# Performance work log

Hardware: AMD Instinct MI355X
Metric: run time of the kernel (lower is better)

The kernel has to match this reference:

```python
import jax, jax.numpy as jnp
import numpy as np

B, C, H, W = 4, 128, 96, 96
INTER = C // 2


def setup_inputs() -> dict:
    key = jax.random.key(0)
    ks = jax.random.split(key, 6)
    scale = 1.0 / np.sqrt(C)
    return {
        "x1": jax.random.normal(ks[0], (B, C, H, W), dtype=jnp.float32),
        "x2": jax.random.normal(ks[1], (B, C, H, W), dtype=jnp.float32),
        "w_theta": jax.random.normal(ks[2], (INTER, C), dtype=jnp.float32) * scale,
        "w_phi": jax.random.normal(ks[3], (INTER, C), dtype=jnp.float32) * scale,
        "w_g": jax.random.normal(ks[4], (INTER, C), dtype=jnp.float32) * scale,
        "w_mask": jax.random.normal(ks[5], (C, INTER), dtype=jnp.float32) * (1.0 / np.sqrt(INTER)),
    }


def reference(x1, x2, w_theta, w_phi, w_g, w_mask):
    b, c, h1, w1 = x1.shape  # c == full channel
    inter = c // 2
    # 1x1 convs (no bias) == channel GEMMs
    theta = jnp.einsum('ic,bchw->bihw', w_theta, x1)   # [b, inter, h1, w1]
    phi   = jnp.einsum('ic,bchw->bihw', w_phi,   x2)   # [b, inter, h2, w2]
    g     = jnp.einsum('ic,bchw->bihw', w_g,     x2)   # [b, inter, h2, w2]
    # Faithful to original: .view(b, c, -1) with c = FULL channel count,
    # so the flattened length is H*W/2 and the contraction dim is c (row-major reshape).
    theta = theta.reshape(b, c, -1).transpose(0, 2, 1)  # [b, N1, c], N1 = h1*w1//2
    phi = phi.reshape(b, c, -1)                         # [b, c, N2]
    g = g.reshape(b, c, -1).transpose(0, 2, 1)          # [b, N2, c]
    scores = jnp.einsum('bnc,bcm->bnm', theta, phi)     # [b, N1, N2]
    attn = jax.nn.softmax(scores, axis=1)               # softmax over dim=1 (query axis!)
    y = jnp.einsum('bnm,bmc->bnc', attn, g)             # [b, N1, c]
    y = y.transpose(0, 2, 1).reshape(b, inter, h1, w1)  # [b, inter, h1, w1]
    mask = jnp.einsum('ci,bihw->bchw', w_mask, y)       # [b, c, h1, w1]
    return mask + x1
```

## Files before the change

### kernel.cpp

```cpp
#include <hip/hip_runtime.h>

typedef __attribute__((ext_vector_type(8))) short short8;
typedef __attribute__((ext_vector_type(4))) float f32x4;
typedef __attribute__((ext_vector_type(16))) float f32x16;
typedef unsigned short u16;
typedef unsigned int u32;

#define NB 4
#define CH 128
#define INTER2 64
#define HW2 9216
#define NN 4608
#define NSLICE 8
#define SLW 576
#define SK 8
#define PCH 136

__device__ __forceinline__ u16 f2bf(float f) {
  u32 u = __float_as_uint(f);
  u += 0x7fffu + ((u >> 16) & 1u);
  return (u16)(u >> 16);
}
__device__ __forceinline__ float bf2f(u16 h) { return __uint_as_float(((u32)h) << 16); }
__device__ __forceinline__ u32 cvtpk(float lo, float hi) {
  u32 r;
  asm("v_cvt_pk_bf16_f32 %0, %1, %2" : "=v"(r) : "v"(lo), "v"(hi));
  return r;
}
__device__ __forceinline__ void gl_lds16(const u16* g, u16* l) {
  __builtin_amdgcn_global_load_lds(
      (const __attribute__((address_space(1))) unsigned int*)g,
      (__attribute__((address_space(3))) unsigned int*)l, 16, 0, 0);
}

__global__ void k_wcvt(const float* __restrict__ wt, const float* __restrict__ wp,
                       const float* __restrict__ wg, const float* __restrict__ wm,
                       u16* __restrict__ wtb, u16* __restrict__ wpb,
                       u16* __restrict__ wgb, u16* __restrict__ wmb) {
  int i = blockIdx.x * 256 + threadIdx.x;
  if (i < CH * INTER2) {
    wtb[i] = f2bf(wt[i]);
    wpb[i] = f2bf(wp[i]);
    wgb[i] = f2bf(wg[i]);
    wmb[i] = f2bf(wm[i]);
  }
}

__global__ __launch_bounds__(256) void k_conv(const float* __restrict__ x1,
                                              const float* __restrict__ x2,
                                              const u16* __restrict__ wtb,
                                              const u16* __restrict__ wpb,
                                              const u16* __restrict__ wgb,
                                              u16* __restrict__ Tt,
                                              u16* __restrict__ Pt,
                                              u16* __restrict__ Gn) {
  __shared__ u16 xT[64 * PCH];
  __shared__ u16 ot[64 * 72];
  const int tid = threadIdx.x;
  const int w = tid >> 6, l = tid & 63, lr = l & 15, lg = l >> 4;
  const int pt = blockIdx.x, b = blockIdx.y, z = blockIdx.z;
  const int p0 = pt * 64;
  const int h = (p0 >= NN) ? 1 : 0;
  const int n0 = p0 - h * NN;
  const float* X = (z ? x2 : x1) + (size_t)b * CH * HW2;

  {
    const int pq = (l & 15) * 4;
    const int cs = w + 4 * (l >> 4);
#pragma unroll
    for (int it = 0; it < 8; it++) {
      const int c = it * 16 + cs;
      float4 v = *(const float4*)(X + (size_t)c * HW2 + p0 + pq);
      xT[(pq + 0) * PCH + c] = f2bf(v.x);
      xT[(pq + 1) * PCH + c] = f2bf(v.y);
      xT[(pq + 2) * PCH + c] = f2bf(v.z);
      xT[(pq + 3) * PCH + c] = f2bf(v.w);
    }
  }
  short8 wsP[4], wsG[4];
  {
    const u16* W1 = z ? wpb : wtb;
#pragma unroll
    for (int ks = 0; ks < 4; ks++)
      wsP[ks] = *(const short8*)(W1 + (w * 16 + lr) * CH + ks * 32 + lg * 8);
    if (z) {
#pragma unroll
      for (int ks = 0; ks < 4; ks++)
        wsG[ks] = *(const short8*)(wgb + (w * 16 + lr) * CH + ks * 32 + lg * 8);
    }
  }
  __syncthreads();
  short8 xf[4][4];
#pragma unroll
  for (int tp = 0; tp < 4; tp++)
#pragma unroll
    for (int ks = 0; ks < 4; ks++)
      xf[tp][ks] = *(const short8*)(&xT[(tp * 16 + lr) * PCH + ks * 32 + lg * 8]);

  f32x4 accP[4];
#pragma unroll
  for (int tp = 0; tp < 4; tp++) {
#pragma unroll
    for (int j = 0; j < 4; j++) accP[tp][j] = 0.f;
#pragma unroll
    for (int ks = 0; ks < 4; ks++)
      accP[tp] = __builtin_amdgcn_mfma_f32_16x16x32_bf16(xf[tp][ks], wsP[ks], accP[tp], 0, 0, 0);
  }
#pragma unroll
  for (int tp = 0; tp < 4; tp++) {
#pragma unroll
    for (int j = 0; j < 4; j++)
      ot[(tp * 16 + lg * 4 + j) * 72 + w * 16 + lr] = f2bf(accP[tp][j]);
  }
  if (z) {
    f32x4 accG[4];
#pragma unroll
    for (int tp = 0; tp < 4; tp++) {
#pragma unroll
      for (int j = 0; j < 4; j++) accG[tp][j] = 0.f;
#pragma unroll
      for (int ks = 0; ks < 4; ks++)
        accG[tp] = __builtin_amdgcn_mfma_f32_16x16x32_bf16(wsG[ks], xf[tp][ks], accG[tp], 0, 0, 0);
    }
    u16* Gb = Gn + (size_t)b * CH * NN;
#pragma unroll
    for (int tp = 0; tp < 4; tp++) {
#pragma unroll
      for (int j = 0; j < 4; j++) {
        const int ig = w * 16 + lg * 4 + j;
        Gb[(size_t)((h << 6) + ig) * NN + n0 + tp * 16 + lr] = f2bf(accG[tp][j]);
      }
    }
  }
  __syncthreads();
  {
    u16* dst = (z ? Pt : Tt) + (size_t)b * NN * CH;
#pragma unroll
    for (int q = 0; q < 2; q++) {
      const int idx = tid * 2 + q;
      const int p = idx >> 3, c8 = (idx & 7) * 8;
      uint4 v = *(const uint4*)(&ot[p * 72 + c8]);
      *(uint4*)(dst + (size_t)(n0 + p) * CH + h * 64 + c8) = v;
    }
  }
}

__global__ __launch_bounds__(256) void k_scores(const u16* __restrict__ Tt,
                                                const u16* __restrict__ Pt,
                                                u16* __restrict__ E,
                                                float* __restrict__ denp,
                                                int b0) {
  const int tid = threadIdx.x;
  const int w = tid >> 6, l = tid & 63, lm = l & 31, lh = l >> 5;
  const int s = blockIdx.x & 7, mt = blockIdx.x >> 3;
  const int eb = blockIdx.y, b = b0 + eb;
  const int m0 = mt * 32;
  const u16* PtB = Pt + (size_t)b * NN * CH;
  const u16* TtB = Tt + (size_t)b * NN * CH;
  u16* Eb = E + (size_t)eb * NN * NN;
  const int nbase = s * SLW;

  short8 bf[8];
#pragma unroll
  for (int ks = 0; ks < 8; ks++)
    bf[ks] = *(const short8*)(PtB + (size_t)(m0 + lm) * CH + ks * 16 + lh * 8);

  float den_l = 0.f;
  short8 ac[8], an[8];
  int tt = w;
#pragma unroll
  for (int ks = 0; ks < 8; ks++)
    ac[ks] = *(const short8*)(TtB + (size_t)(nbase + tt * 32 + lm) * CH + ks * 16 + lh * 8);
  for (; tt < 18; tt += 4) {
    const int tn = tt + 4;
    if (tn < 18) {
#pragma unroll
      for (int ks = 0; ks < 8; ks++)
        an[ks] = *(const short8*)(TtB + (size_t)(nbase + tn * 32 + lm) * CH + ks * 16 + lh * 8);
    }
    f32x16 acc;
#pragma unroll
    for (int q = 0; q < 16; q++) acc[q] = 0.f;
#pragma unroll
    for (int ks = 0; ks < 8; ks++)
      acc = __builtin_amdgcn_mfma_f32_32x32x16_bf16(ac[ks], bf[ks], acc, 0, 0, 0);
    const int nb = nbase + tt * 32;
#pragma unroll
    for (int q = 0; q < 16; q += 2) {
      const int n = nb + (q & 3) + 8 * (q >> 2) + 4 * lh;
      float e0 = exp2f(__builtin_fmaf(acc[q], 1.44269504f, -57.70780163f));
      float e1 = exp2f(__builtin_fmaf(acc[q + 1], 1.44269504f, -57.70780163f));
      den_l += e0;
      den_l += e1;
      u32 pk = cvtpk(e0, e1);
      Eb[(size_t)n * NN + m0 + lm] = (u16)pk;
      Eb[(size_t)(n + 1) * NN + m0 + lm] = (u16)(pk >> 16);
    }
    if (tn < 18) {
#pragma unroll
      for (int ks = 0; ks < 8; ks++) ac[ks] = an[ks];
    }
  }
  den_l += __shfl_xor(den_l, 32, 64);
  __shared__ float dl[4][32];
  if (l < 32) dl[w][l] = den_l;
  __syncthreads();
  if (tid < 32)
    denp[(size_t)(s * NB + b) * NN + m0 + tid] =
        dl[0][tid] + dl[1][tid] + dl[2][tid] + dl[3][tid];
}

__global__ __launch_bounds__(256) void k_gd(const u16* __restrict__ Gn,
                                            const float* __restrict__ denp,
                                            u16* __restrict__ Gd,
                                            int b0) {
  const int q = blockIdx.x * 256 + threadIdx.x;
  const int d = q / 576, mc = q % 576;
  const int m0 = mc * 8;
  const int b = b0 + blockIdx.y;
  float dn[8];
#pragma unroll
  for (int i = 0; i < 8; i++) dn[i] = 0.f;
#pragma unroll
  for (int s = 0; s < NSLICE; s++) {
    const float* dp = denp + (size_t)(s * NB + b) * NN + m0;
    float4 a = *(const float4*)dp;
    float4 c = *(const float4*)(dp + 4);
    dn[0] += a.x; dn[1] += a.y; dn[2] += a.z; dn[3] += a.w;
    dn[4] += c.x; dn[5] += c.y; dn[6] += c.z; dn[7] += c.w;
  }
  const size_t off = (size_t)b * CH * NN + (size_t)d * NN + m0;
  uint4 v = *(const uint4*)(Gn + off);
  u32 arr[4] = {v.x, v.y, v.z, v.w};
  uint4 o;
  u32 ov[4];
#pragma unroll
  for (int j = 0; j < 4; j++) {
    float lo = bf2f((u16)(arr[j] & 0xffffu)) / dn[2 * j];
    float hi = bf2f((u16)(arr[j] >> 16)) / dn[2 * j + 1];
    ov[j] = cvtpk(lo, hi);
  }
  o.x = ov[0]; o.y = ov[1]; o.z = ov[2]; o.w = ov[3];
  *(uint4*)(Gd + off) = o;
}

__global__ __launch_bounds__(256) void k_pv(const u16* __restrict__ E,
                                            const u16* __restrict__ Gd,
                                            float* __restrict__ Yp,
                                            int b0) {
  __shared__ u16 lA[128 * 64];
  __shared__ u16 lB[128 * 64];
  const int tid = threadIdx.x;
  const int w = tid >> 6, l = tid & 63, lr = l & 15, lg = l >> 4;
  const int sk = blockIdx.x / 36, nt = blockIdx.x % 36;
  const int eb = blockIdx.y, b = b0 + eb;
  const int n0 = nt * 128;
  const int k0 = sk * (NN / SK);
  const u16* Eb = E + (size_t)eb * NN * NN;
  const u16* Gb = Gd + (size_t)b * CH * NN;
  const int wm = w >> 1, wn2 = w & 1;
  const int rl = l >> 3;
  const int cg = (l & 7) ^ rl;

  f32x4 acc[4][4];
#pragma unroll
  for (int fa = 0; fa < 4; fa++)
#pragma unroll
    for (int fb = 0; fb < 4; fb++)
#pragma unroll
      for (int j = 0; j < 4; j++) acc[fa][fb][j] = 0.f;

#define STAGE(kk)                                                                   \
  {                                                                                 \
    _Pragma("unroll") for (int r = 0; r < 4; r++) {                                 \
      const int rowA = r * 32 + w * 8 + rl;                                         \
      gl_lds16(Gb + (size_t)rowA * NN + (kk) + cg * 8, &lA[(r * 32 + w * 8) * 64]); \
      gl_lds16(Eb + (size_t)(n0 + rowA) * NN + (kk) + cg * 8,                       \
               &lB[(r * 32 + w * 8) * 64]);                                         \
    }                                                                               \
  }

  STAGE(k0);
  const int NKS = (NN / SK) / 64;
  for (int st = 0; st < NKS; st++) {
    __syncthreads();
#pragma unroll
    for (int ks2 = 0; ks2 < 2; ks2++) {
      const int cw = ((ks2 * 4 + lg) ^ (lr & 7)) * 8;
      short8 af[4], bfr[4];
#pragma unroll
      for (int fa = 0; fa < 4; fa++)
        af[fa] = *(const short8*)(&lA[(wm * 64 + fa * 16 + lr) * 64 + cw]);
#pragma unroll
      for (int fb = 0; fb < 4; fb++)
        bfr[fb] = *(const short8*)(&lB[(wn2 * 64 + fb * 16 + lr) * 64 + cw]);
#pragma unroll
      for (int fa = 0; fa < 4; fa++)
#pragma unroll
        for (int fb = 0; fb < 4; fb++)
          acc[fa][fb] = __builtin_amdgcn_mfma_f32_16x16x32_bf16(af[fa], bfr[fb], acc[fa][fb], 0, 0, 0);
    }
    __syncthreads();
    if (st + 1 < NKS) STAGE(k0 + (st + 1) * 64);
  }
#undef STAGE
  const int slab = sk * 2 + eb;
  float* Yb = Yp + (size_t)slab * CH * NN;
#pragma unroll
  for (int fa = 0; fa < 4; fa++) {
#pragma unroll
    for (int fb = 0; fb < 4; fb++) {
      const int n = n0 + wn2 * 64 + fb * 16 + lr;
#pragma unroll
      for (int j = 0; j < 4; j++) {
        const int cc = wm * 64 + fa * 16 + lg * 4 + j;
        Yb[(size_t)cc * NN + n] = acc[fa][fb][j];
      }
    }
  }
}

__global__ __launch_bounds__(256) void k_out(const float* __restrict__ Yp,
                                             const u16* __restrict__ wmb,
                                             const float* __restrict__ x1,
                                             float* __restrict__ out,
                                             int b0) {
  __shared__ u16 yy[64][72];
  const int tid = threadIdx.x;
  const int w = tid >> 6, l = tid & 63, lr = l & 15, lg = l >> 4;
  const int eb = blockIdx.y, b = b0 + eb;
  const int n0 = blockIdx.x * 32;
  const int nl = tid & 31, cch = tid >> 5;

  float v[16];
#pragma unroll
  for (int q = 0; q < 16; q++) v[q] = 0.f;
  for (int s2 = 0; s2 < SK; s2++) {
    const float* base = Yp + ((size_t)(s2 * 2 + eb) * CH + cch * 16) * NN + n0 + nl;
#pragma unroll
    for (int q = 0; q < 16; q++) v[q] += base[(size_t)q * NN];
  }
#pragma unroll
  for (int q = 0; q < 16; q++) {
    const int d = cch * 16 + q;
    yy[(d >> 6) * 32 + nl][d & 63] = f2bf(v[q]);
  }
  __syncthreads();

  const int wm3 = w >> 1, wp3 = w & 1;
  f32x4 eacc[4][2];
#pragma unroll
  for (int fa = 0; fa < 4; fa++)
#pragma unroll
    for (int fb = 0; fb < 2; fb++)
#pragma unroll
      for (int j = 0; j < 4; j++) eacc[fa][fb][j] = 0.f;
#pragma unroll
  for (int ks = 0; ks < 2; ks++) {
    short8 wa[4];
#pragma unroll
    for (int fa = 0; fa < 4; fa++)
      wa[fa] = *(const short8*)(wmb + (wm3 * 64 + fa * 16 + lr) * 64 + ks * 32 + lg * 8);
    short8 yb[2];
#pragma unroll
    for (int fb = 0; fb < 2; fb++)
      yb[fb] = *(const short8*)(&yy[wp3 * 32 + fb * 16 + lr][ks * 32 + lg * 8]);
#pragma unroll
    for (int fa = 0; fa < 4; fa++)
#pragma unroll
      for (int fb = 0; fb < 2; fb++)
        eacc[fa][fb] = __builtin_amdgcn_mfma_f32_16x16x32_bf16(wa[fa], yb[fb], eacc[fa][fb], 0, 0, 0);
  }
  const float* x1b = x1 + (size_t)b * CH * HW2;
  float* ob = out + (size_t)b * CH * HW2;
#pragma unroll
  for (int fa = 0; fa < 4; fa++) {
#pragma unroll
    for (int fb = 0; fb < 2; fb++) {
      const int pl = wp3 * 32 + fb * 16 + lr;
      const int col = n0 + (pl & 31) + (pl >> 5) * NN;
#pragma unroll
      for (int j = 0; j < 4; j++) {
        const int c = wm3 * 64 + fa * 16 + lg * 4 + j;
        const size_t o = (size_t)c * HW2 + col;
        ob[o] = eacc[fa][fb][j] + x1b[o];
      }
    }
  }
}

extern "C" void kernel_launch(void* const* d_in, const int* in_sizes, int n_in,
                              void* d_out, int out_size, void* d_ws, size_t ws_size,
                              hipStream_t stream) {
  const float* x1 = (const float*)d_in[0];
  const float* x2 = (const float*)d_in[1];
  const float* wt = (const float*)d_in[2];
  const float* wp = (const float*)d_in[3];
  const float* wg = (const float*)d_in[4];
  const float* wm = (const float*)d_in[5];
  float* out = (float*)d_out;

  char* ws = (char*)d_ws;
  const size_t SZ_T = (size_t)NB * NN * CH * 2;
  u16* Tt = (u16*)ws; ws += SZ_T;
  u16* Pt = (u16*)ws; ws += SZ_T;
  u16* Gn = (u16*)ws; ws += SZ_T;
  u16* Gd = (u16*)ws; ws += SZ_T;
  float* denp = (float*)ws; ws += (size_t)NSLICE * NB * NN * 4;
  u16* wtb = (u16*)ws; ws += (size_t)CH * INTER2 * 2;
  u16* wpb = (u16*)ws; ws += (size_t)CH * INTER2 * 2;
  u16* wgb = (u16*)ws; ws += (size_t)CH * INTER2 * 2;
  u16* wmb = (u16*)ws; ws += (size_t)CH * INTER2 * 2;
  float* Yp = (float*)ws; ws += (size_t)16 * CH * NN * 4;
  u16* E = (u16*)ws;

  const size_t fixed = (size_t)(ws - (char*)d_ws);
  const size_t eslab = (size_t)NN * NN * 2;
  int eslots = 0;
  if (ws_size >= fixed + 2 * eslab) eslots = 2;
  else if (ws_size >= fixed + 1 * eslab) eslots = 1;
  if (eslots == 0) return;

  hipLaunchKernelGGL(k_wcvt, dim3(32), dim3(256), 0, stream, wt, wp, wg, wm, wtb, wpb, wgb, wmb);
  hipLaunchKernelGGL(k_conv, dim3(144, NB, 2), dim3(256), 0, stream, x1, x2, wtb, wpb, wgb, Tt, Pt, Gn);
  for (int b0 = 0; b0 < NB; b0 += eslots) {
    hipLaunchKernelGGL(k_scores, dim3(144 * 8, eslots), dim3(256), 0, stream, Tt, Pt, E, denp, b0);
    hipLaunchKernelGGL(k_gd, dim3(288, eslots), dim3(256), 0, stream, Gn, denp, Gd, b0);
    hipLaunchKernelGGL(k_pv, dim3(SK * 36, eslots), dim3(256), 0, stream, E, Gd, Yp, b0);
    hipLaunchKernelGGL(k_out, dim3(144, eslots), dim3(256), 0, stream, Yp, wmb, x1, out, b0);
  }
}
```

Before: 209.1 us.

## Stage score tile in LDS for coalesced E writes with 64x64 blocks

```diff
diff --git a/kernel.cpp b/kernel.cpp
--- a/kernel.cpp
+++ b/kernel.cpp
@@ -150,33 +150,35 @@
                                                 u16* __restrict__ E,
                                                 float* __restrict__ denp,
                                                 int b0) {
+  __shared__ u16 Et[64 * 72];
   const int tid = threadIdx.x;
   const int w = tid >> 6, l = tid & 63, lm = l & 31, lh = l >> 5;
+  const int wm2 = w >> 1, wn2 = w & 1;
   const int s = blockIdx.x & 7, mt = blockIdx.x >> 3;
   const int eb = blockIdx.y, b = b0 + eb;
-  const int m0 = mt * 32;
+  const int m0 = mt * 64;
+  const int nbase = s * SLW;
   const u16* PtB = Pt + (size_t)b * NN * CH;
   const u16* TtB = Tt + (size_t)b * NN * CH;
   u16* Eb = E + (size_t)eb * NN * NN;
-  const int nbase = s * SLW;
 
   short8 bf[8];
 #pragma unroll
   for (int ks = 0; ks < 8; ks++)
-    bf[ks] = *(const short8*)(PtB + (size_t)(m0 + lm) * CH + ks * 16 + lh * 8);
+    bf[ks] = *(const short8*)(PtB + (size_t)(m0 + wm2 * 32 + lm) * CH + ks * 16 + lh * 8);
 
   float den_l = 0.f;
   short8 ac[8], an[8];
-  int tt = w;
 #pragma unroll
   for (int ks = 0; ks < 8; ks++)
-    ac[ks] = *(const short8*)(TtB + (size_t)(nbase + tt * 32 + lm) * CH + ks * 16 + lh * 8);
-  for (; tt < 18; tt += 4) {
-    const int tn = tt + 4;
-    if (tn < 18) {
+    ac[ks] = *(const short8*)(TtB + (size_t)(nbase + wn2 * 32 + lm) * CH + ks * 16 + lh * 8);
+
+  for (int it = 0; it < 9; it++) {
+    if (it + 1 < 9) {
+      const int nr = nbase + (it + 1) * 64 + wn2 * 32 + lm;
 #pragma unroll
       for (int ks = 0; ks < 8; ks++)
-        an[ks] = *(const short8*)(TtB + (size_t)(nbase + tn * 32 + lm) * CH + ks * 16 + lh * 8);
+        an[ks] = *(const short8*)(TtB + (size_t)nr * CH + ks * 16 + lh * 8);
     }
     f32x16 acc;
 #pragma unroll
@@ -184,19 +186,30 @@
 #pragma unroll
     for (int ks = 0; ks < 8; ks++)
       acc = __builtin_amdgcn_mfma_f32_32x32x16_bf16(ac[ks], bf[ks], acc, 0, 0, 0);
-    const int nb = nbase + tt * 32;
 #pragma unroll
     for (int q = 0; q < 16; q += 2) {
-      const int n = nb + (q & 3) + 8 * (q >> 2) + 4 * lh;
+      const int nl = wn2 * 32 + (q & 3) + 8 * (q >> 2) + 4 * lh;
       float e0 = exp2f(__builtin_fmaf(acc[q], 1.44269504f, -57.70780163f));
       float e1 = exp2f(__builtin_fmaf(acc[q + 1], 1.44269504f, -57.70780163f));
       den_l += e0;
       den_l += e1;
       u32 pk = cvtpk(e0, e1);
-      Eb[(size_t)n * NN + m0 + lm] = (u16)pk;
-      Eb[(size_t)(n + 1) * NN + m0 + lm] = (u16)(pk >> 16);
-    }
-    if (tn < 18) {
+      Et[nl * 72 + wm2 * 32 + lm] = (u16)pk;
+      Et[(nl + 1) * 72 + wm2 * 32 + lm] = (u16)(pk >> 16);
+    }
+    __syncthreads();
+    {
+      const int row0 = tid >> 3, col = (tid & 7) * 8;
+      const int ng = nbase + it * 64;
+#pragma unroll
+      for (int p = 0; p < 2; p++) {
+        const int r2 = p * 32 + row0;
+        uint4 v = *(const uint4*)(&Et[r2 * 72 + col]);
+        *(uint4*)(Eb + (size_t)(ng + r2) * NN + m0 + col) = v;
+      }
+    }
+    __syncthreads();
+    if (it + 1 < 9) {
 #pragma unroll
       for (int ks = 0; ks < 8; ks++) ac[ks] = an[ks];
     }
@@ -205,9 +218,9 @@
   __shared__ float dl[4][32];
   if (l < 32) dl[w][l] = den_l;
   __syncthreads();
-  if (tid < 32)
+  if (tid < 64)
     denp[(size_t)(s * NB + b) * NN + m0 + tid] =
-        dl[0][tid] + dl[1][tid] + dl[2][tid] + dl[3][tid];
+        dl[(tid >> 5) * 2][tid & 31] + dl[(tid >> 5) * 2 + 1][tid & 31];
 }
 
 __global__ __launch_bounds__(256) void k_gd(const u16* __restrict__ Gn,
@@ -424,7 +437,7 @@
   hipLaunchKernelGGL(k_wcvt, dim3(32), dim3(256), 0, stream, wt, wp, wg, wm, wtb, wpb, wgb, wmb);
   hipLaunchKernelGGL(k_conv, dim3(144, NB, 2), dim3(256), 0, stream, x1, x2, wtb, wpb, wgb, Tt, Pt, Gn);
   for (int b0 = 0; b0 < NB; b0 += eslots) {
-    hipLaunchKernelGGL(k_scores, dim3(144 * 8, eslots), dim3(256), 0, stream, Tt, Pt, E, denp, b0);
+    hipLaunchKernelGGL(k_scores, dim3(72 * 8, eslots), dim3(256), 0, stream, Tt, Pt, E, denp, b0);
     hipLaunchKernelGGL(k_gd, dim3(288, eslots), dim3(256), 0, stream, Gn, denp, Gd, b0);
     hipLaunchKernelGGL(k_pv, dim3(SK * 36, eslots), dim3(256), 0, stream, E, Gd, Yp, b0);
     hipLaunchKernelGGL(k_out, dim3(144, eslots), dim3(256), 0, stream, Yp, wmb, x1, out, b0);
```

After: 204.5 us. 1.02x faster.
